# Optimization experiments

Hardware: AMD Instinct MI355X
Metric: run time of the kernel (lower is better)

Reference implementation:

```python
import jax, jax.numpy as jnp
import numpy as np

D = 1024
H = 8
DK = D // H
BS, NSEG, NSEN = 16, 64, 32


def _linear_params(key, d_in, d_out, scale=0.02):
    kw, kb = jax.random.split(key)
    w = jax.random.normal(kw, (d_out, d_in), dtype=jnp.float32) * scale
    b = jax.random.normal(kb, (d_out,), dtype=jnp.float32) * scale
    return w, b


def setup_inputs() -> dict:
    key = jax.random.key(0)
    ks = jax.random.split(key, 12)
    A = jax.random.normal(ks[0], (BS, NSEG, D), dtype=jnp.float32)
    V = jax.random.normal(ks[1], (BS, NSEG, D), dtype=jnp.float32)
    S = jax.random.normal(ks[2], (BS, NSEN, D), dtype=jnp.float32)
    wA, bA = _linear_params(ks[3], D, D)
    wV, bV = _linear_params(ks[4], D, D)
    wS, bS = _linear_params(ks[5], D, D)
    wq, bq = _linear_params(ks[6], D, D)
    wk, bk = _linear_params(ks[7], D, D)
    wv, bv = _linear_params(ks[8], D, D)
    w1, b1 = _linear_params(ks[9], D, D)
    w2, b2 = _linear_params(ks[10], D, D)
    return {"A": A, "V": V, "S": S,
            "wA": wA, "bA": bA, "wV": wV, "bV": bV, "wS": wS, "bS": bS,
            "wq": wq, "bq": bq, "wk": wk, "bk": bk, "wv": wv, "bv": bv,
            "w1": w1, "b1": b1, "w2": w2, "b2": b2}


def _lin(x, w, b):
    return x @ w.T + b


def reference(A, V, S, wA, bA, wV, bV, wS, bS, wq, bq, wk, bk, wv, bv, w1, b1, w2, b2):
    bs, num_seg, d_model = A.shape
    num_sen = S.shape[1]
    A = _lin(A, wA, bA)
    V = _lin(V, wV, bV)
    S = _lin(S, wS, bS)
    av = jnp.stack([A, V], axis=2)                       # (bs, num_seg, 2, d)
    q = _lin(S, wq, bq).reshape(bs, num_sen, H, DK)      # (b, s, h, dk)
    k = _lin(av, wk, bk).reshape(bs, num_seg, 2, H, DK)  # (b, g, a, h, dk)
    v = _lin(av, wv, bv).reshape(bs, num_seg, 2, H, DK)
    # attention over the size-2 A/V axis only
    attn = jnp.einsum('bshd,bgahd->bsgah', q, k) / np.sqrt(DK).astype(np.float32)
    attn = jax.nn.softmax(attn, axis=3)                  # softmax over a (A vs V)
    out = jnp.einsum('bsgah,bgahd->bsghd', attn, v)
    out = out.reshape(bs, num_sen, num_seg, d_model)
    # positionwise FF: Linear -> ReLU -> Linear (dropout p=0)
    out = _lin(jax.nn.relu(_lin(out, w1, b1)), w2, b2)
    return out
```

## Files before the change

### kernel.cpp

```cpp
#include <hip/hip_runtime.h>
#include <stdint.h>


#define D_MODEL 1024
#define N_HEAD  8
#define DK      128
#define BS      16
#define NSEG    64
#define NSEN    32

typedef __attribute__((ext_vector_type(8))) __bf16 bf16x8;
typedef __attribute__((ext_vector_type(8))) unsigned short u16x8;
typedef __attribute__((ext_vector_type(4))) float f32x4;

__device__ __forceinline__ float bf2f(unsigned short b) {
  union { unsigned int u; float f; } x; x.u = ((unsigned int)b) << 16; return x.f;
}
__device__ __forceinline__ unsigned short f2bf(float f) {
  union { float f; unsigned int u; } x; x.f = f;
  unsigned int u = x.u;
  unsigned int r = (u + 0x7fffu + ((u >> 16) & 1u)) >> 16;
  return (unsigned short)r;
}

__device__ __forceinline__ void g2l16(const void* g, void* l) {
  __builtin_amdgcn_global_load_lds(
      (const __attribute__((address_space(1))) void*)g,
      (__attribute__((address_space(3))) void*)l, 16, 0, 0);
}

struct CvtB { const float* s[11]; unsigned short* d[11]; int n4[11]; };
__global__ __launch_bounds__(256)
void cvtall_kernel(CvtB p) {
  const int z = blockIdx.y;
  const int i = blockIdx.x * 256 + threadIdx.x;
  if (i >= p.n4[z]) return;
  float4 v = reinterpret_cast<const float4*>(p.s[z])[i];
  ushort4 o;
  o.x = f2bf(v.x); o.y = f2bf(v.y); o.z = f2bf(v.z); o.w = f2bf(v.w);
  reinterpret_cast<ushort4*>(p.d[z])[i] = o;
}

struct GSeg { const unsigned short* A; const unsigned short* B;
              const float* bias; unsigned short* C; };
struct GBatch { GSeg s[3]; int end[3]; };

__global__ __launch_bounds__(256)
void gemm64_bt(GBatch gb) {
  __shared__ __align__(16) unsigned short lA[2][64 * 32];
  __shared__ __align__(16) unsigned short lB[2][128 * 32];

  const int nwg = gridDim.x;
  const int sw = (blockIdx.x & 7) * (nwg >> 3) + (blockIdx.x >> 3);
  int sgi = 0, base = 0;
  if (sw >= gb.end[0]) { sgi = 1; base = gb.end[0]; }
  if (sw >= gb.end[1]) { sgi = 2; base = gb.end[1]; }
  const GSeg sg = gb.s[sgi];
  const int st = sw - base;
  const int m0 = (st >> 3) * 64, n0 = (st & 7) * 128;

  const int t = threadIdx.x;
  const int lane = t & 63, w = t >> 6;
  const int fr = lane & 15, kg = lane >> 4;

  f32x4 acc[2][4] = {};

  const int r  = t >> 2;
  const int c8 = (t & 3) * 8;
  const unsigned short* ga  = sg.A + (size_t)(m0 + r) * 1024 + c8;
  const unsigned short* gbp = sg.B + (size_t)(n0 + r) * 1024 + c8;

  auto stage = [&](int buf, int k0) {
    g2l16(ga + k0,              &lA[buf][t * 8]);
    g2l16(gbp + k0,             &lB[buf][t * 8]);
    g2l16(gbp + k0 + 64 * 1024, &lB[buf][2048 + t * 8]);
  };

  stage(0, 0);
  asm volatile("s_waitcnt vmcnt(0)" ::: "memory");
  __syncthreads();

  for (int k0 = 0; k0 < 1024; k0 += 32) {
    const int buf = (k0 >> 5) & 1;
    if (k0 + 32 < 1024) stage(buf ^ 1, k0 + 32);

    u16x8 af[4], bf[2];
#pragma unroll
    for (int mi = 0; mi < 4; ++mi)
      af[mi] = *reinterpret_cast<const u16x8*>(&lA[buf][(mi * 16 + fr) * 32 + kg * 8]);
#pragma unroll
    for (int ni = 0; ni < 2; ++ni)
      bf[ni] = *reinterpret_cast<const u16x8*>(&lB[buf][(w * 32 + ni * 16 + fr) * 32 + kg * 8]);
#pragma unroll
    for (int ni = 0; ni < 2; ++ni)
#pragma unroll
      for (int mi = 0; mi < 4; ++mi)
        acc[ni][mi] = __builtin_amdgcn_mfma_f32_16x16x32_bf16(
            __builtin_bit_cast(bf16x8, bf[ni]), __builtin_bit_cast(bf16x8, af[mi]),
            acc[ni][mi], 0, 0, 0);

    asm volatile("s_waitcnt vmcnt(0)" ::: "memory");
    __syncthreads();
  }

#pragma unroll
  for (int ni = 0; ni < 2; ++ni) {
    const int gn0 = n0 + w * 32 + ni * 16 + kg * 4;
    const float4 bv = *reinterpret_cast<const float4*>(&sg.bias[gn0]);
#pragma unroll
    for (int mi = 0; mi < 4; ++mi) {
      const int gm = m0 + mi * 16 + fr;
      ushort4 o;
      o.x = f2bf(acc[ni][mi][0] + bv.x);
      o.y = f2bf(acc[ni][mi][1] + bv.y);
      o.z = f2bf(acc[ni][mi][2] + bv.z);
      o.w = f2bf(acc[ni][mi][3] + bv.w);
      *reinterpret_cast<ushort4*>(&sg.C[(size_t)gm * 1024 + gn0]) = o;
    }
  }
}

__global__ __launch_bounds__(512, 4)
void ff2_gemm(const unsigned short* __restrict__ A, const unsigned short* __restrict__ B,
              const float* __restrict__ bias, float* __restrict__ C,
              int M, int N, int K) {
  __shared__ __align__(16) unsigned short lds[2 * 12288];

  const int nwg = gridDim.x;
  const int sw = (blockIdx.x & 7) * (nwg >> 3) + (blockIdx.x >> 3);
  const int m0 = (sw >> 3) * 256, n0 = (sw & 7) * 128;

  const int T = threadIdx.x;
  const int lane = T & 63, wave = T >> 6;
  const int wr = wave >> 1, wc = wave & 1;
  const int fr = lane & 15, kg = lane >> 4;
  const int NT = K >> 5;

  char* ldsc = (char*)lds;

  const int srow = T >> 2;
  const int gsl = ((T & 3) ^ ((srow & 3) ^ ((srow >> 2) & 3))) * 8;
  const unsigned short* A0 = A + (size_t)(m0 + srow) * K + gsl;
  const unsigned short* A1 = A + (size_t)(m0 + 128 + srow) * K + gsl;
  const unsigned short* B0 = B + (size_t)(n0 + srow) * K + gsl;

  auto stage = [&](int buf, int t) {
    const int kb = t * 32;
    char* dst = ldsc + buf * 24576 + T * 16;
    g2l16(A0 + kb, dst);
    g2l16(A1 + kb, dst + 8192);
    g2l16(B0 + kb, dst + 16384);
  };

  int raddr[4], baddr[4];
#pragma unroll
  for (int mi = 0; mi < 4; ++mi) {
    int lr = wr * 64 + mi * 16 + fr;
    raddr[mi] = lr * 64 + ((kg ^ ((lr & 3) ^ ((lr >> 2) & 3))) * 16);
  }
#pragma unroll
  for (int ni = 0; ni < 4; ++ni) {
    int lr = wc * 64 + ni * 16 + fr;
    baddr[ni] = 16384 + lr * 64 + ((kg ^ ((lr & 3) ^ ((lr >> 2) & 3))) * 16);
  }

  f32x4 acc[4][4] = {};

  stage(0, 0);
  asm volatile("s_waitcnt vmcnt(0)" ::: "memory");
  __builtin_amdgcn_s_barrier();

  for (int t = 0; t < NT; ++t) {
    const int buf = t & 1;
    if (t + 1 < NT) stage(buf ^ 1, t + 1);

    const char* base = ldsc + buf * 24576;
    u16x8 af[4], bf[4];
#pragma unroll
    for (int mi = 0; mi < 4; ++mi)
      af[mi] = *reinterpret_cast<const u16x8*>(base + raddr[mi]);
#pragma unroll
    for (int ni = 0; ni < 4; ++ni)
      bf[ni] = *reinterpret_cast<const u16x8*>(base + baddr[ni]);

    __builtin_amdgcn_s_setprio(1);
#pragma unroll
    for (int ni = 0; ni < 4; ++ni)
#pragma unroll
      for (int mi = 0; mi < 4; ++mi)
        acc[ni][mi] = __builtin_amdgcn_mfma_f32_16x16x32_bf16(
            __builtin_bit_cast(bf16x8, bf[ni]), __builtin_bit_cast(bf16x8, af[mi]),
            acc[ni][mi], 0, 0, 0);
    __builtin_amdgcn_s_setprio(0);

    asm volatile("s_waitcnt vmcnt(0)" ::: "memory");
    __builtin_amdgcn_s_barrier();
  }

#pragma unroll
  for (int ni = 0; ni < 4; ++ni) {
    const int gn0 = n0 + wc * 64 + ni * 16 + kg * 4;
    const float4 bv = *reinterpret_cast<const float4*>(&bias[gn0]);
#pragma unroll
    for (int mi = 0; mi < 4; ++mi) {
      const int gm = m0 + wr * 64 + mi * 16 + fr;
      float4 o;
      o.x = acc[ni][mi][0] + bv.x;
      o.y = acc[ni][mi][1] + bv.y;
      o.z = acc[ni][mi][2] + bv.z;
      o.w = acc[ni][mi][3] + bv.w;
      *reinterpret_cast<float4*>(&C[(size_t)gm * N + gn0]) = o;
    }
  }
}

__global__ __launch_bounds__(256)
void uav_gemm(const unsigned short* __restrict__ vAV, const unsigned short* __restrict__ w1,
              unsigned short* __restrict__ UAV) {
  __shared__ __align__(16) unsigned short lA[2][128 * 32];
  __shared__ __align__(16) unsigned short lB[2][128 * 32];

  const int zb = blockIdx.z;
  const int tensor = zb >> 3, h = zb & 7;
  const unsigned short* Ab = vAV + (size_t)tensor * (1024 * 1024) + h * 128;
  const unsigned short* Bb = w1 + h * 128;
  unsigned short* Cb = UAV + (size_t)tensor * (1024 * 8192) + h * 1024;

  const int t = threadIdx.x;
  const int m0 = blockIdx.y * 128, n0 = blockIdx.x * 128;
  const int lane = t & 63, wv = t >> 6;
  const int wrow = (wv >> 1) * 64, wcol = (wv & 1) * 64;
  const int fr = lane & 15, kg = lane >> 4;

  f32x4 acc[4][4] = {};

  const int r  = t >> 2;
  const int c8 = (t & 3) * 8;
  const unsigned short* ga = Ab + (size_t)(m0 + r) * 1024 + c8;
  const unsigned short* gb = Bb + (size_t)(n0 + r) * 1024 + c8;

  auto stage = [&](int buf, int k0) {
    g2l16(ga + k0,             &lA[buf][t * 8]);
    g2l16(ga + k0 + 64 * 1024, &lA[buf][2048 + t * 8]);
    g2l16(gb + k0,             &lB[buf][t * 8]);
    g2l16(gb + k0 + 64 * 1024, &lB[buf][2048 + t * 8]);
  };

  stage(0, 0);
  asm volatile("s_waitcnt vmcnt(0)" ::: "memory");
  __syncthreads();

  for (int k0 = 0; k0 < 128; k0 += 32) {
    const int buf = (k0 >> 5) & 1;
    if (k0 + 32 < 128) stage(buf ^ 1, k0 + 32);

    u16x8 af[4], bg_[4];
#pragma unroll
    for (int mi = 0; mi < 4; ++mi)
      af[mi] = *reinterpret_cast<const u16x8*>(&lA[buf][(wrow + mi * 16 + fr) * 32 + kg * 8]);
#pragma unroll
    for (int ni = 0; ni < 4; ++ni)
      bg_[ni] = *reinterpret_cast<const u16x8*>(&lB[buf][(wcol + ni * 16 + fr) * 32 + kg * 8]);
#pragma unroll
    for (int ni = 0; ni < 4; ++ni)
#pragma unroll
      for (int mi = 0; mi < 4; ++mi)
        acc[ni][mi] = __builtin_amdgcn_mfma_f32_16x16x32_bf16(
            __builtin_bit_cast(bf16x8, bg_[ni]), __builtin_bit_cast(bf16x8, af[mi]),
            acc[ni][mi], 0, 0, 0);

    asm volatile("s_waitcnt vmcnt(0)" ::: "memory");
    __syncthreads();
  }

#pragma unroll
  for (int ni = 0; ni < 4; ++ni) {
    const int gn0 = n0 + wcol + ni * 16 + kg * 4;
#pragma unroll
    for (int mi = 0; mi < 4; ++mi) {
      const int gm = m0 + wrow + mi * 16 + fr;
      ushort4 o;
      o.x = f2bf(acc[ni][mi][0]);
      o.y = f2bf(acc[ni][mi][1]);
      o.z = f2bf(acc[ni][mi][2]);
      o.w = f2bf(acc[ni][mi][3]);
      *reinterpret_cast<ushort4*>(&Cb[(size_t)gm * 8192 + gn0]) = o;
    }
  }
}

__global__ __launch_bounds__(256)
void score_hid_kernel(const unsigned short* __restrict__ q,
                      const unsigned short* __restrict__ kAV,
                      const unsigned short* __restrict__ UAV,
                      const float* __restrict__ b1,
                      unsigned short* __restrict__ hid) {
  const int bg = blockIdx.x;
  const int b = bg >> 6, g = bg & 63;
  __shared__ float sk[2][D_MODEL];
  __shared__ float pAl[NSEN][N_HEAD];
  const size_t rowA = (size_t)bg * D_MODEL;
  const size_t rowV = rowA + (size_t)BS * NSEG * D_MODEL;
  for (int i = threadIdx.x; i < D_MODEL; i += 256) {
    sk[0][i] = bf2f(kAV[rowA + i]);
    sk[1][i] = bf2f(kAV[rowV + i]);
  }
  __syncthreads();

  const int h = threadIdx.x >> 5;
  const int l = threadIdx.x & 31;
  const float scale = 0.08838834764831845f;

  for (int s = 0; s < NSEN; ++s) {
    const unsigned short* pq = q + ((size_t)(b * NSEN + s)) * D_MODEL + h * DK;
    float la = 0.f, lv = 0.f;
#pragma unroll
    for (int e = 0; e < 4; ++e) {
      int d = l + e * 32;
      float qv = bf2f(pq[d]);
      la += qv * sk[0][h * DK + d];
      lv += qv * sk[1][h * DK + d];
    }
#pragma unroll
    for (int off = 16; off; off >>= 1) {
      la += __shfl_xor(la, off, 32);
      lv += __shfl_xor(lv, off, 32);
    }
    if (l == 0) pAl[s][h] = 1.f / (1.f + __expf((lv - la) * scale));
  }
  __syncthreads();

  const int n0 = threadIdx.x * 4;
  const unsigned short* ua = UAV + (size_t)bg * 8192 + n0;
  const unsigned short* uv = ua + (size_t)1024 * 8192;

  float dU[N_HEAD][4];
  float base[4];
#pragma unroll
  for (int j = 0; j < 4; ++j) base[j] = b1[n0 + j];
#pragma unroll
  for (int hh = 0; hh < N_HEAD; ++hh) {
    ushort4 a4 = *reinterpret_cast<const ushort4*>(ua + hh * 1024);
    ushort4 v4 = *reinterpret_cast<const ushort4*>(uv + hh * 1024);
    float va[4] = {bf2f(a4.x), bf2f(a4.y), bf2f(a4.z), bf2f(a4.w)};
    float vv[4] = {bf2f(v4.x), bf2f(v4.y), bf2f(v4.z), bf2f(v4.w)};
#pragma unroll
    for (int j = 0; j < 4; ++j) { dU[hh][j] = va[j] - vv[j]; base[j] += vv[j]; }
  }

  for (int s = 0; s < NSEN; ++s) {
    float val[4] = {base[0], base[1], base[2], base[3]};
#pragma unroll
    for (int hh = 0; hh < N_HEAD; ++hh) {
      const float p = pAl[s][hh];
#pragma unroll
      for (int j = 0; j < 4; ++j) val[j] = fmaf(p, dU[hh][j], val[j]);
    }
    ushort4 o;
    o.x = f2bf(val[0] > 0.f ? val[0] : 0.f);
    o.y = f2bf(val[1] > 0.f ? val[1] : 0.f);
    o.z = f2bf(val[2] > 0.f ? val[2] : 0.f);
    o.w = f2bf(val[3] > 0.f ? val[3] : 0.f);
    size_t orow = ((size_t)(b * NSEN + s) * NSEG + g) * D_MODEL + n0;
    *reinterpret_cast<ushort4*>(hid + orow) = o;
  }
}

extern "C" void kernel_launch(void* const* d_in, const int* in_sizes, int n_in,
                              void* d_out, int out_size, void* d_ws, size_t ws_size,
                              hipStream_t stream) {
  const float* A  = (const float*)d_in[0];
  const float* V  = (const float*)d_in[1];
  const float* S  = (const float*)d_in[2];
  const float* wA = (const float*)d_in[3];  const float* bA = (const float*)d_in[4];
  const float* wV = (const float*)d_in[5];  const float* bV = (const float*)d_in[6];
  const float* wS = (const float*)d_in[7];  const float* bS = (const float*)d_in[8];
  const float* wq = (const float*)d_in[9];  const float* bq = (const float*)d_in[10];
  const float* wk = (const float*)d_in[11]; const float* bk = (const float*)d_in[12];
  const float* wv = (const float*)d_in[13]; const float* bv = (const float*)d_in[14];
  const float* w1 = (const float*)d_in[15]; const float* b1 = (const float*)d_in[16];
  const float* w2 = (const float*)d_in[17]; const float* b2 = (const float*)d_in[18];

  const int nAV = BS * NSEG * D_MODEL;
  const int nS  = BS * NSEN * D_MODEL;
  const int nW  = D_MODEL * D_MODEL;
  const int nCT = BS * NSEN * NSEG * D_MODEL;
  const int nU  = 2 * 1024 * 8 * 1024;

  char* ws = (char*)d_ws;
  size_t off = 0;
  auto carve = [&](size_t elems) {
    unsigned short* p = (unsigned short*)(ws + off);
    off += elems * sizeof(unsigned short);
    return p;
  };
  unsigned short* bwA = carve(nW);
  unsigned short* bwV = carve(nW);
  unsigned short* bwS = carve(nW);
  unsigned short* bwq = carve(nW);
  unsigned short* bwk = carve(nW);
  unsigned short* bwv = carve(nW);
  unsigned short* bw1 = carve(nW);
  unsigned short* bw2 = carve(nW);
  unsigned short* xA  = carve(nAV);
  unsigned short* xV  = carve(nAV);
  unsigned short* xS  = carve(nS);
  unsigned short* A1V1 = carve(2 * nAV);
  unsigned short* S1  = carve(nS);
  unsigned short* qb  = carve(nS);
  unsigned short* kAV = carve(2 * nAV);
  unsigned short* vAV = carve(2 * nAV);
  unsigned short* UAV = carve(nU);
  unsigned short* hid = carve(nCT);
  (void)ws_size; (void)n_in; (void)in_sizes; (void)out_size;

  CvtB cv;
  cv.s[0] = wA; cv.d[0] = bwA; cv.n4[0] = nW / 4;
  cv.s[1] = wV; cv.d[1] = bwV; cv.n4[1] = nW / 4;
  cv.s[2] = wS; cv.d[2] = bwS; cv.n4[2] = nW / 4;
  cv.s[3] = wq; cv.d[3] = bwq; cv.n4[3] = nW / 4;
  cv.s[4] = wk; cv.d[4] = bwk; cv.n4[4] = nW / 4;
  cv.s[5] = wv; cv.d[5] = bwv; cv.n4[5] = nW / 4;
  cv.s[6] = w1; cv.d[6] = bw1; cv.n4[6] = nW / 4;
  cv.s[7] = w2; cv.d[7] = bw2; cv.n4[7] = nW / 4;
  cv.s[8] = A;  cv.d[8] = xA;  cv.n4[8] = nAV / 4;
  cv.s[9] = V;  cv.d[9] = xV;  cv.n4[9] = nAV / 4;
  cv.s[10] = S; cv.d[10] = xS; cv.n4[10] = nS / 4;
  cvtall_kernel<<<dim3(1024, 11), dim3(256), 0, stream>>>(cv);

  GBatch pj;
  pj.s[0] = {xA, bwA, bA, A1V1};        pj.end[0] = 128;
  pj.s[1] = {xV, bwV, bV, A1V1 + nAV};  pj.end[1] = 256;
  pj.s[2] = {xS, bwS, bS, S1};          pj.end[2] = 320;
  gemm64_bt<<<dim3(320), 256, 0, stream>>>(pj);

  GBatch qkv;
  qkv.s[0] = {S1,   bwq, bq, qb};   qkv.end[0] = 64;
  qkv.s[1] = {A1V1, bwk, bk, kAV};  qkv.end[1] = 320;
  qkv.s[2] = {A1V1, bwv, bv, vAV};  qkv.end[2] = 576;
  gemm64_bt<<<dim3(576), 256, 0, stream>>>(qkv);

  uav_gemm<<<dim3(8, 8, 16), dim3(256), 0, stream>>>(vAV, bw1, UAV);

  score_hid_kernel<<<dim3(BS * NSEG), dim3(256), 0, stream>>>(qb, kAV, UAV, b1, hid);

  ff2_gemm<<<dim3(1024), 512, 0, stream>>>(hid, bw2, b2, (float*)d_out,
                                           32768, 1024, 1024);
}
```

Baseline: 211.2 us.

## Triple-buffer GEMM pipelines and enlarge FF2 tile to 256x256

```diff
diff --git a/kernel.cpp b/kernel.cpp
--- a/kernel.cpp
+++ b/kernel.cpp
@@ -47,8 +47,7 @@
 
 __global__ __launch_bounds__(256)
 void gemm64_bt(GBatch gb) {
-  __shared__ __align__(16) unsigned short lA[2][64 * 32];
-  __shared__ __align__(16) unsigned short lB[2][128 * 32];
+  __shared__ __align__(16) unsigned short lds[3 * 6144];
 
   const int nwg = gridDim.x;
   const int sw = (blockIdx.x & 7) * (nwg >> 3) + (blockIdx.x >> 3);
@@ -69,28 +68,37 @@
   const int c8 = (t & 3) * 8;
   const unsigned short* ga  = sg.A + (size_t)(m0 + r) * 1024 + c8;
   const unsigned short* gbp = sg.B + (size_t)(n0 + r) * 1024 + c8;
+  char* ldsc = (char*)lds;
 
   auto stage = [&](int buf, int k0) {
-    g2l16(ga + k0,              &lA[buf][t * 8]);
-    g2l16(gbp + k0,             &lB[buf][t * 8]);
-    g2l16(gbp + k0 + 64 * 1024, &lB[buf][2048 + t * 8]);
+    char* d = ldsc + buf * 12288;
+    g2l16(ga + k0,              d + t * 16);
+    g2l16(gbp + k0,             d + 4096 + t * 16);
+    g2l16(gbp + k0 + 64 * 1024, d + 8192 + t * 16);
   };
 
   stage(0, 0);
-  asm volatile("s_waitcnt vmcnt(0)" ::: "memory");
-  __syncthreads();
-
-  for (int k0 = 0; k0 < 1024; k0 += 32) {
-    const int buf = (k0 >> 5) & 1;
-    if (k0 + 32 < 1024) stage(buf ^ 1, k0 + 32);
-
+  stage(1, 32);
+
+  const int NT = 32;
+  for (int it = 0; it < NT; ++it) {
+    if (it < NT - 1) asm volatile("s_waitcnt vmcnt(3)" ::: "memory");
+    else             asm volatile("s_waitcnt vmcnt(0)" ::: "memory");
+    __builtin_amdgcn_s_barrier();
+
+    const char* bufp = ldsc + (it % 3) * 12288;
     u16x8 af[4], bf[2];
 #pragma unroll
     for (int mi = 0; mi < 4; ++mi)
-      af[mi] = *reinterpret_cast<const u16x8*>(&lA[buf][(mi * 16 + fr) * 32 + kg * 8]);
+      af[mi] = *reinterpret_cast<const u16x8*>(bufp + (mi * 16 + fr) * 64 + kg * 16);
 #pragma unroll
     for (int ni = 0; ni < 2; ++ni)
-      bf[ni] = *reinterpret_cast<const u16x8*>(&lB[buf][(w * 32 + ni * 16 + fr) * 32 + kg * 8]);
+      bf[ni] = *reinterpret_cast<const u16x8*>(bufp + 4096 + (w * 32 + ni * 16 + fr) * 64 + kg * 16);
+
+    if (it + 2 < NT) stage((it + 2) % 3, (it + 2) * 32);
+    __builtin_amdgcn_sched_barrier(0);
+
+    __builtin_amdgcn_s_setprio(1);
 #pragma unroll
     for (int ni = 0; ni < 2; ++ni)
 #pragma unroll
@@ -98,9 +106,7 @@
         acc[ni][mi] = __builtin_amdgcn_mfma_f32_16x16x32_bf16(
             __builtin_bit_cast(bf16x8, bf[ni]), __builtin_bit_cast(bf16x8, af[mi]),
             acc[ni][mi], 0, 0, 0);
-
-    asm volatile("s_waitcnt vmcnt(0)" ::: "memory");
-    __syncthreads();
+    __builtin_amdgcn_s_setprio(0);
   }
 
 #pragma unroll
@@ -120,19 +126,19 @@
   }
 }
 
-__global__ __launch_bounds__(512, 4)
+__global__ __launch_bounds__(512, 2)
 void ff2_gemm(const unsigned short* __restrict__ A, const unsigned short* __restrict__ B,
               const float* __restrict__ bias, float* __restrict__ C,
               int M, int N, int K) {
-  __shared__ __align__(16) unsigned short lds[2 * 12288];
+  __shared__ __align__(16) unsigned short lds[3 * 16384];
 
   const int nwg = gridDim.x;
   const int sw = (blockIdx.x & 7) * (nwg >> 3) + (blockIdx.x >> 3);
-  const int m0 = (sw >> 3) * 256, n0 = (sw & 7) * 128;
+  const int m0 = (sw >> 2) * 256, n0 = (sw & 3) * 256;
 
   const int T = threadIdx.x;
   const int lane = T & 63, wave = T >> 6;
-  const int wr = wave >> 1, wc = wave & 1;
+  const int wr = wave >> 2, wc = wave & 3;
   const int fr = lane & 15, kg = lane >> 4;
   const int NT = K >> 5;
 
@@ -143,58 +149,60 @@
   const unsigned short* A0 = A + (size_t)(m0 + srow) * K + gsl;
   const unsigned short* A1 = A + (size_t)(m0 + 128 + srow) * K + gsl;
   const unsigned short* B0 = B + (size_t)(n0 + srow) * K + gsl;
-
-  auto stage = [&](int buf, int t) {
-    const int kb = t * 32;
-    char* dst = ldsc + buf * 24576 + T * 16;
-    g2l16(A0 + kb, dst);
-    g2l16(A1 + kb, dst + 8192);
-    g2l16(B0 + kb, dst + 16384);
+  const unsigned short* B1 = B + (size_t)(n0 + 128 + srow) * K + gsl;
+
+  auto stage = [&](int buf, int tt) {
+    const int kb = tt * 32;
+    char* d = ldsc + buf * 32768 + T * 16;
+    g2l16(A0 + kb, d);
+    g2l16(A1 + kb, d + 8192);
+    g2l16(B0 + kb, d + 16384);
+    g2l16(B1 + kb, d + 24576);
   };
 
-  int raddr[4], baddr[4];
-#pragma unroll
-  for (int mi = 0; mi < 4; ++mi) {
-    int lr = wr * 64 + mi * 16 + fr;
-    raddr[mi] = lr * 64 + ((kg ^ ((lr & 3) ^ ((lr >> 2) & 3))) * 16);
+  int raddr[8], baddr[4];
+#pragma unroll
+  for (int mi = 0; mi < 8; ++mi) {
+    int ra = wr * 128 + mi * 16 + fr;
+    raddr[mi] = ra * 64 + ((kg ^ ((ra & 3) ^ ((ra >> 2) & 3))) * 16);
   }
 #pragma unroll
   for (int ni = 0; ni < 4; ++ni) {
-    int lr = wc * 64 + ni * 16 + fr;
-    baddr[ni] = 16384 + lr * 64 + ((kg ^ ((lr & 3) ^ ((lr >> 2) & 3))) * 16);
-  }
-
-  f32x4 acc[4][4] = {};
+    int rb = wc * 64 + ni * 16 + fr;
+    baddr[ni] = 16384 + rb * 64 + ((kg ^ ((rb & 3) ^ ((rb >> 2) & 3))) * 16);
+  }
+
+  f32x4 acc[4][8] = {};
 
   stage(0, 0);
-  asm volatile("s_waitcnt vmcnt(0)" ::: "memory");
-  __builtin_amdgcn_s_barrier();
+  stage(1, 1);
 
   for (int t = 0; t < NT; ++t) {
-    const int buf = t & 1;
-    if (t + 1 < NT) stage(buf ^ 1, t + 1);
-
-    const char* base = ldsc + buf * 24576;
-    u16x8 af[4], bf[4];
-#pragma unroll
-    for (int mi = 0; mi < 4; ++mi)
-      af[mi] = *reinterpret_cast<const u16x8*>(base + raddr[mi]);
+    if (t < NT - 1) asm volatile("s_waitcnt vmcnt(4)" ::: "memory");
+    else            asm volatile("s_waitcnt vmcnt(0)" ::: "memory");
+    __builtin_amdgcn_s_barrier();
+
+    const char* bufp = ldsc + (t % 3) * 32768;
+    u16x8 af[8], bf[4];
+#pragma unroll
+    for (int mi = 0; mi < 8; ++mi)
+      af[mi] = *reinterpret_cast<const u16x8*>(bufp + raddr[mi]);
 #pragma unroll
     for (int ni = 0; ni < 4; ++ni)
-      bf[ni] = *reinterpret_cast<const u16x8*>(base + baddr[ni]);
+      bf[ni] = *reinterpret_cast<const u16x8*>(bufp + baddr[ni]);
+
+    if (t + 2 < NT) stage((t + 2) % 3, t + 2);
+    __builtin_amdgcn_sched_barrier(0);
 
     __builtin_amdgcn_s_setprio(1);
 #pragma unroll
     for (int ni = 0; ni < 4; ++ni)
 #pragma unroll
-      for (int mi = 0; mi < 4; ++mi)
+      for (int mi = 0; mi < 8; ++mi)
         acc[ni][mi] = __builtin_amdgcn_mfma_f32_16x16x32_bf16(
             __builtin_bit_cast(bf16x8, bf[ni]), __builtin_bit_cast(bf16x8, af[mi]),
             acc[ni][mi], 0, 0, 0);
     __builtin_amdgcn_s_setprio(0);
-
-    asm volatile("s_waitcnt vmcnt(0)" ::: "memory");
-    __builtin_amdgcn_s_barrier();
   }
 
 #pragma unroll
@@ -202,8 +210,8 @@
     const int gn0 = n0 + wc * 64 + ni * 16 + kg * 4;
     const float4 bv = *reinterpret_cast<const float4*>(&bias[gn0]);
 #pragma unroll
-    for (int mi = 0; mi < 4; ++mi) {
-      const int gm = m0 + wr * 64 + mi * 16 + fr;
+    for (int mi = 0; mi < 8; ++mi) {
+      const int gm = m0 + wr * 128 + mi * 16 + fr;
       float4 o;
       o.x = acc[ni][mi][0] + bv.x;
       o.y = acc[ni][mi][1] + bv.y;
@@ -444,6 +452,6 @@
 
   score_hid_kernel<<<dim3(BS * NSEG), dim3(256), 0, stream>>>(qb, kAV, UAV, b1, hid);
 
-  ff2_gemm<<<dim3(1024), 512, 0, stream>>>(hid, bw2, b2, (float*)d_out,
-                                           32768, 1024, 1024);
-}
+  ff2_gemm<<<dim3(512), 512, 0, stream>>>(hid, bw2, b2, (float*)d_out,
+                                          32768, 1024, 1024);
+}
```

Result: faster. 198.9 us (-5.8%).

## Use 128x128 tiles with triple-buffered swizzled LDS in projection GEMMs

Applied to the files above, without the earlier changes.

```diff
diff --git a/kernel.cpp b/kernel.cpp
--- a/kernel.cpp
+++ b/kernel.cpp
@@ -45,10 +45,9 @@
               const float* bias; unsigned short* C; };
 struct GBatch { GSeg s[3]; int end[3]; };
 
-__global__ __launch_bounds__(256)
-void gemm64_bt(GBatch gb) {
-  __shared__ __align__(16) unsigned short lA[2][64 * 32];
-  __shared__ __align__(16) unsigned short lB[2][128 * 32];
+__global__ __launch_bounds__(256, 3)
+void gemm128_bt(GBatch gb) {
+  __shared__ __align__(16) unsigned short lds[3 * 8192];
 
   const int nwg = gridDim.x;
   const int sw = (blockIdx.x & 7) * (nwg >> 3) + (blockIdx.x >> 3);
@@ -57,59 +56,100 @@
   if (sw >= gb.end[1]) { sgi = 2; base = gb.end[1]; }
   const GSeg sg = gb.s[sgi];
   const int st = sw - base;
-  const int m0 = (st >> 3) * 64, n0 = (st & 7) * 128;
-
-  const int t = threadIdx.x;
-  const int lane = t & 63, w = t >> 6;
+  const int m0 = (st >> 3) * 128, n0 = (st & 7) * 128;
+
+  const int T = threadIdx.x;
+  const int lane = T & 63, wave = T >> 6;
+  const int wr = wave >> 1, wc = wave & 1;
   const int fr = lane & 15, kg = lane >> 4;
 
-  f32x4 acc[2][4] = {};
-
-  const int r  = t >> 2;
-  const int c8 = (t & 3) * 8;
-  const unsigned short* ga  = sg.A + (size_t)(m0 + r) * 1024 + c8;
-  const unsigned short* gbp = sg.B + (size_t)(n0 + r) * 1024 + c8;
+  char* ldsc = (char*)lds;
+
+  const int srow = T >> 2;
+  const int gsl = ((T & 3) ^ ((srow & 3) ^ ((srow >> 2) & 3))) * 8;
+  const unsigned short* A0 = sg.A + (size_t)(m0 + srow) * 1024 + gsl;
+  const unsigned short* A1 = sg.A + (size_t)(m0 + 64 + srow) * 1024 + gsl;
+  const unsigned short* B0 = sg.B + (size_t)(n0 + srow) * 1024 + gsl;
+  const unsigned short* B1 = sg.B + (size_t)(n0 + 64 + srow) * 1024 + gsl;
 
   auto stage = [&](int buf, int k0) {
-    g2l16(ga + k0,              &lA[buf][t * 8]);
-    g2l16(gbp + k0,             &lB[buf][t * 8]);
-    g2l16(gbp + k0 + 64 * 1024, &lB[buf][2048 + t * 8]);
+    char* d = ldsc + buf * 16384;
+    g2l16(A0 + k0, d + T * 16);
+    g2l16(A1 + k0, d + 4096 + T * 16);
+    g2l16(B0 + k0, d + 8192 + T * 16);
+    g2l16(B1 + k0, d + 12288 + T * 16);
   };
 
+  int raddr[4], baddr[4];
+#pragma unroll
+  for (int mi = 0; mi < 4; ++mi) {
+    int ra = wr * 64 + mi * 16 + fr;
+    raddr[mi] = ra * 64 + ((kg ^ ((ra & 3) ^ ((ra >> 2) & 3))) * 16);
+  }
+#pragma unroll
+  for (int ni = 0; ni < 4; ++ni) {
+    int rb = wc * 64 + ni * 16 + fr;
+    baddr[ni] = 8192 + rb * 64 + ((kg ^ ((rb & 3) ^ ((rb >> 2) & 3))) * 16);
+  }
+
+  f32x4 acc[4][4] = {};
+  u16x8 f0[8], f1[8];
+
+#define G128_LOAD(DST, BUF)                                                    \
+  {                                                                            \
+    const char* bp_ = ldsc + (BUF) * 16384;                                    \
+    _Pragma("unroll")                                                          \
+    for (int mi = 0; mi < 4; ++mi)                                             \
+      DST[mi] = *reinterpret_cast<const u16x8*>(bp_ + raddr[mi]);              \
+    _Pragma("unroll")                                                          \
+    for (int ni = 0; ni < 4; ++ni)                                             \
+      DST[4 + ni] = *reinterpret_cast<const u16x8*>(bp_ + baddr[ni]);          \
+  }
+
+#define G128_MFMA(SRC)                                                         \
+  {                                                                            \
+    __builtin_amdgcn_s_setprio(1);                                             \
+    _Pragma("unroll")                                                          \
+    for (int ni = 0; ni < 4; ++ni)                                             \
+      _Pragma("unroll")                                                        \
+      for (int mi = 0; mi < 4; ++mi)                                           \
+        acc[ni][mi] = __builtin_amdgcn_mfma_f32_16x16x32_bf16(                 \
+            __builtin_bit_cast(bf16x8, SRC[4 + ni]),                           \
+            __builtin_bit_cast(bf16x8, SRC[mi]), acc[ni][mi], 0, 0, 0);        \
+    __builtin_amdgcn_s_setprio(0);                                             \
+  }
+
+#define G128_ITER(T_, CUR, NXT)                                                \
+  {                                                                            \
+    if ((T_) + 2 < NT) stage(((T_) + 2) % 3, ((T_) + 2) * 32);                 \
+    if ((T_) + 1 < NT) {                                                       \
+      if ((T_) + 2 < NT) asm volatile("s_waitcnt vmcnt(4)" ::: "memory");      \
+      else               asm volatile("s_waitcnt vmcnt(0)" ::: "memory");      \
+      __builtin_amdgcn_s_barrier();                                            \
+      G128_LOAD(NXT, ((T_) + 1) % 3);                                          \
+    }                                                                          \
+    G128_MFMA(CUR);                                                            \
+  }
+
+  const int NT = 32;
   stage(0, 0);
-  asm volatile("s_waitcnt vmcnt(0)" ::: "memory");
-  __syncthreads();
-
-  for (int k0 = 0; k0 < 1024; k0 += 32) {
-    const int buf = (k0 >> 5) & 1;
-    if (k0 + 32 < 1024) stage(buf ^ 1, k0 + 32);
-
-    u16x8 af[4], bf[2];
-#pragma unroll
-    for (int mi = 0; mi < 4; ++mi)
-      af[mi] = *reinterpret_cast<const u16x8*>(&lA[buf][(mi * 16 + fr) * 32 + kg * 8]);
-#pragma unroll
-    for (int ni = 0; ni < 2; ++ni)
-      bf[ni] = *reinterpret_cast<const u16x8*>(&lB[buf][(w * 32 + ni * 16 + fr) * 32 + kg * 8]);
-#pragma unroll
-    for (int ni = 0; ni < 2; ++ni)
-#pragma unroll
-      for (int mi = 0; mi < 4; ++mi)
-        acc[ni][mi] = __builtin_amdgcn_mfma_f32_16x16x32_bf16(
-            __builtin_bit_cast(bf16x8, bf[ni]), __builtin_bit_cast(bf16x8, af[mi]),
-            acc[ni][mi], 0, 0, 0);
-
-    asm volatile("s_waitcnt vmcnt(0)" ::: "memory");
-    __syncthreads();
-  }
-
-#pragma unroll
-  for (int ni = 0; ni < 2; ++ni) {
-    const int gn0 = n0 + w * 32 + ni * 16 + kg * 4;
+  stage(1, 32);
+  asm volatile("s_waitcnt vmcnt(4)" ::: "memory");
+  __builtin_amdgcn_s_barrier();
+  G128_LOAD(f0, 0);
+
+  for (int it = 0; it < NT; it += 2) {
+    G128_ITER(it,     f0, f1);
+    G128_ITER(it + 1, f1, f0);
+  }
+
+#pragma unroll
+  for (int ni = 0; ni < 4; ++ni) {
+    const int gn0 = n0 + wc * 64 + ni * 16 + kg * 4;
     const float4 bv = *reinterpret_cast<const float4*>(&sg.bias[gn0]);
 #pragma unroll
     for (int mi = 0; mi < 4; ++mi) {
-      const int gm = m0 + mi * 16 + fr;
+      const int gm = m0 + wr * 64 + mi * 16 + fr;
       ushort4 o;
       o.x = f2bf(acc[ni][mi][0] + bv.x);
       o.y = f2bf(acc[ni][mi][1] + bv.y);
@@ -330,39 +370,41 @@
   }
   __syncthreads();
 
-  const int n0 = threadIdx.x * 4;
-  const unsigned short* ua = UAV + (size_t)bg * 8192 + n0;
+  const int tn = (threadIdx.x & 127) * 8;
+  const int sb = (threadIdx.x >> 7) * 16;
+  const unsigned short* ua = UAV + (size_t)bg * 8192 + tn;
   const unsigned short* uv = ua + (size_t)1024 * 8192;
 
-  float dU[N_HEAD][4];
-  float base[4];
-#pragma unroll
-  for (int j = 0; j < 4; ++j) base[j] = b1[n0 + j];
+  float dU[N_HEAD][8];
+  float base[8];
+#pragma unroll
+  for (int j = 0; j < 8; ++j) base[j] = b1[tn + j];
 #pragma unroll
   for (int hh = 0; hh < N_HEAD; ++hh) {
-    ushort4 a4 = *reinterpret_cast<const ushort4*>(ua + hh * 1024);
-    ushort4 v4 = *reinterpret_cast<const ushort4*>(uv + hh * 1024);
-    float va[4] = {bf2f(a4.x), bf2f(a4.y), bf2f(a4.z), bf2f(a4.w)};
-    float vv[4] = {bf2f(v4.x), bf2f(v4.y), bf2f(v4.z), bf2f(v4.w)};
-#pragma unroll
-    for (int j = 0; j < 4; ++j) { dU[hh][j] = va[j] - vv[j]; base[j] += vv[j]; }
-  }
-
-  for (int s = 0; s < NSEN; ++s) {
-    float val[4] = {base[0], base[1], base[2], base[3]};
+    u16x8 a8 = *reinterpret_cast<const u16x8*>(ua + hh * 1024);
+    u16x8 v8 = *reinterpret_cast<const u16x8*>(uv + hh * 1024);
+#pragma unroll
+    for (int j = 0; j < 8; ++j) {
+      float va = bf2f(a8[j]), vv = bf2f(v8[j]);
+      dU[hh][j] = va - vv; base[j] += vv;
+    }
+  }
+
+  for (int s = sb; s < sb + 16; ++s) {
+    float val[8];
+#pragma unroll
+    for (int j = 0; j < 8; ++j) val[j] = base[j];
 #pragma unroll
     for (int hh = 0; hh < N_HEAD; ++hh) {
       const float p = pAl[s][hh];
 #pragma unroll
-      for (int j = 0; j < 4; ++j) val[j] = fmaf(p, dU[hh][j], val[j]);
-    }
-    ushort4 o;
-    o.x = f2bf(val[0] > 0.f ? val[0] : 0.f);
-    o.y = f2bf(val[1] > 0.f ? val[1] : 0.f);
-    o.z = f2bf(val[2] > 0.f ? val[2] : 0.f);
-    o.w = f2bf(val[3] > 0.f ? val[3] : 0.f);
-    size_t orow = ((size_t)(b * NSEN + s) * NSEG + g) * D_MODEL + n0;
-    *reinterpret_cast<ushort4*>(hid + orow) = o;
+      for (int j = 0; j < 8; ++j) val[j] = fmaf(p, dU[hh][j], val[j]);
+    }
+    u16x8 o;
+#pragma unroll
+    for (int j = 0; j < 8; ++j) o[j] = f2bf(val[j] > 0.f ? val[j] : 0.f);
+    size_t orow = ((size_t)(b * NSEN + s) * NSEG + g) * D_MODEL + tn;
+    *reinterpret_cast<u16x8*>(hid + orow) = o;
   }
 }
 
@@ -429,16 +471,16 @@
   cvtall_kernel<<<dim3(1024, 11), dim3(256), 0, stream>>>(cv);
 
   GBatch pj;
-  pj.s[0] = {xA, bwA, bA, A1V1};        pj.end[0] = 128;
-  pj.s[1] = {xV, bwV, bV, A1V1 + nAV};  pj.end[1] = 256;
-  pj.s[2] = {xS, bwS, bS, S1};          pj.end[2] = 320;
-  gemm64_bt<<<dim3(320), 256, 0, stream>>>(pj);
+  pj.s[0] = {xA, bwA, bA, A1V1};        pj.end[0] = 64;
+  pj.s[1] = {xV, bwV, bV, A1V1 + nAV};  pj.end[1] = 128;
+  pj.s[2] = {xS, bwS, bS, S1};          pj.end[2] = 160;
+  gemm128_bt<<<dim3(160), 256, 0, stream>>>(pj);
 
   GBatch qkv;
-  qkv.s[0] = {S1,   bwq, bq, qb};   qkv.end[0] = 64;
-  qkv.s[1] = {A1V1, bwk, bk, kAV};  qkv.end[1] = 320;
-  qkv.s[2] = {A1V1, bwv, bv, vAV};  qkv.end[2] = 576;
-  gemm64_bt<<<dim3(576), 256, 0, stream>>>(qkv);
+  qkv.s[0] = {S1,   bwq, bq, qb};   qkv.end[0] = 32;
+  qkv.s[1] = {A1V1, bwk, bk, kAV};  qkv.end[1] = 160;
+  qkv.s[2] = {A1V1, bwv, bv, vAV};  qkv.end[2] = 288;
+  gemm128_bt<<<dim3(288), 256, 0, stream>>>(qkv);
 
   uav_gemm<<<dim3(8, 8, 16), dim3(256), 0, stream>>>(vAV, bw1, UAV);
 
```

Measured after the change: 209.4 us. Within noise of the previous version (-0.9%).
